# Optimization experiments

Hardware: AMD Instinct MI355X
Metric: run time of the kernel (lower is better)

## Reference

```python
import jax, jax.numpy as jnp
import numpy as np

ALPHA = 0.5
SIGMA = 1.0
THRESH = 0.1
MAX_THIN_ITERS = 128


def _gaussian_kernel(sigma):
    # scipy.ndimage.gaussian_filter default: truncate=4.0 -> radius = int(4*sigma+0.5)
    radius = int(4.0 * sigma + 0.5)
    x = np.arange(-radius, radius + 1, dtype=np.float64)
    k = np.exp(-0.5 * (x / sigma) ** 2)
    k = k / k.sum()
    return jnp.asarray(k.astype(np.float32)), radius


def _blur1d(x, k, r, axis):
    # separable Gaussian along `axis`, scipy mode='reflect' == numpy 'symmetric'
    pad = [(0, 0)] * x.ndim
    pad[axis] = (r, r)
    xp = jnp.pad(x, pad, mode='symmetric')
    n = x.shape[axis]
    out = jnp.zeros_like(x)
    for i in range(2 * r + 1):
        out = out + k[i] * jax.lax.slice_in_dim(xp, i, i + n, axis=axis)
    return out


def gaussian_blur(img, sigma):  # img: [B, H, W]
    k, r = _gaussian_kernel(sigma)
    return _blur1d(_blur1d(img, k, r, axis=1), k, r, axis=2)


def _shift(x, dy, dx):
    # neighbor value x[i+dy, j+dx] brought to [i, j], zero-padded border
    B, H, W = x.shape
    xp = jnp.pad(x, ((0, 0), (1, 1), (1, 1)))
    return xp[:, 1 + dy:1 + dy + H, 1 + dx:1 + dx + W]


def _zs_substep(img, step):
    # Zhang-Suen thinning sub-iteration; img is float {0,1} [B, H, W]
    # P2..P9 clockwise starting at north
    P = [_shift(img, -1, 0), _shift(img, -1, 1), _shift(img, 0, 1), _shift(img, 1, 1),
         _shift(img, 1, 0), _shift(img, 1, -1), _shift(img, 0, -1), _shift(img, -1, -1)]
    Bn = P[0]
    for p in P[1:]:
        Bn = Bn + p
    seq = P + [P[0]]
    A = jnp.zeros_like(img)
    for i in range(8):
        A = A + ((seq[i] < 0.5) & (seq[i + 1] > 0.5)).astype(img.dtype)
    p2, p3, p4, p5, p6, p7, p8, p9 = P
    if step == 0:
        c1 = (p2 * p4 * p6) < 0.5
        c2 = (p4 * p6 * p8) < 0.5
    else:
        c1 = (p2 * p4 * p8) < 0.5
        c2 = (p2 * p6 * p8) < 0.5
    delete = (img > 0.5) & (Bn >= 2) & (Bn <= 6) & (A == 1) & c1 & c2
    return jnp.where(delete, jnp.zeros_like(img), img)


def skeletonize(binary):  # binary float {0,1} [B, H, W] -> thinned skeleton
    def body(state):
        img, _, it = state
        img2 = _zs_substep(_zs_substep(img, 0), 1)
        return img2, jnp.any(img2 != img), it + 1

    def cond(state):
        return state[1] & (state[2] < MAX_THIN_ITERS)

    img, _, _ = jax.lax.while_loop(cond, body, (binary, jnp.array(True), jnp.array(0)))
    return img


def create_centerline_mask(gt2d, sigma=SIGMA, threshold=THRESH):  # [B, H, W]
    smooth = gaussian_blur(gt2d, sigma)
    binary = (smooth > threshold).astype(jnp.float32)
    return skeletonize(binary)


def setup_inputs() -> dict:
    key = jax.random.key(0)
    k1, k2, k3 = jax.random.split(key, 3)
    B, N, H, W = 2, 8, 512, 512
    gt = (jax.random.uniform(k2, (B, N, H, W)) > 0.9).astype(jnp.float32)
    pred = gt + 0.1 * jax.random.normal(k1, (B, N, H, W), dtype=jnp.float32)
    return {"pred_projections": pred, "gt_projections": gt}


def reference(pred_projections, gt_projections):
    B, N, H, W = pred_projections.shape
    pred = pred_projections.reshape(B * N, H, W)
    gt = gt_projections.reshape(B * N, H, W)
    # mask is built from gt only (torch detaches before CPU round-trip)
    mask = create_centerline_mask(jax.lax.stop_gradient(gt))
    diff = pred - gt
    l2_loss = jnp.mean(diff ** 2)            # == mean over per-projection mse_loss
    cl_loss = jnp.mean((diff * mask) ** 2)   # == mean over per-projection masked mse
    return ALPHA * l2_loss + (1.0 - ALPHA) * cl_loss
```

## Files before the change

kernel.cpp:

```cpp
#include <hip/hip_runtime.h>
#include <stdint.h>
#include <math.h>

static constexpr int NIMG  = 16;
static constexpr int HH    = 512;
static constexpr int WW    = 512;
static constexpr int TOTAL = NIMG * HH * WW;
static constexpr int WPR   = WW / 64;
static constexpr int QPI   = HH * WPR;
static constexpr int NQ    = TOTAL / 64;
static constexpr int MAXIT = 128;
static constexpr int SW    = 9;
static constexpr int RBLK  = 1024;

static constexpr size_t OFF_PACK = 0;
static constexpr size_t OFF_PART = (size_t)NQ * 8;

__device__ __forceinline__ void make_gk(float* gks) {
    if (threadIdx.x < 9) {
        double ssum = 0.0;
        for (int i = 0; i < 9; ++i) { double x = (double)(i - 4); ssum += exp(-0.5 * x * x); }
        double x = (double)((int)threadIdx.x - 4);
        gks[threadIdx.x] = (float)(exp(-0.5 * x * x) / ssum);
    }
}

__global__ void __launch_bounds__(256) fused_blur(const float* __restrict__ gt,
                                                  uint64_t* __restrict__ packed) {
    __shared__ float tin[72 * 72];
    __shared__ float tv[64 * 72];
    __shared__ float gks[9];
    const int tid = threadIdx.x;
    make_gk(gks);
    const int img  = blockIdx.x >> 6;
    const int tile = blockIdx.x & 63;
    const int oy = (tile >> 3) << 6, ox = (tile & 7) << 6;
    const float* G = gt + (size_t)img * (HH * WW);
    for (int i = tid; i < 72 * 72; i += 256) {
        int r = i / 72, c = i - r * 72;
        int gy = oy - 4 + r, gx = ox - 4 + c;
        gy = gy < 0 ? -gy - 1 : (gy >= HH ? 2 * HH - 1 - gy : gy);
        gx = gx < 0 ? -gx - 1 : (gx >= WW ? 2 * WW - 1 - gx : gx);
        tin[i] = G[gy * WW + gx];
    }
    __syncthreads();
    for (int i = tid; i < 64 * 72; i += 256) {
        int r = i / 72, c = i - r * 72;
        float s = 0.f;
#pragma unroll
        for (int t = 0; t < 9; ++t) s += gks[t] * tin[(r + t) * 72 + c];
        tv[i] = s;
    }
    __syncthreads();
    const int lane = tid & 63, w = tid >> 6;
    for (int j = 0; j < 16; ++j) {
        int yr = w * 16 + j;
        float s = 0.f;
#pragma unroll
        for (int t = 0; t < 9; ++t) s += gks[t] * tv[yr * 72 + lane + t];
        uint64_t m = __ballot(s > 0.1f);
        if (lane == 0) packed[(size_t)img * QPI + (oy + yr) * WPR + (ox >> 6)] = m;
    }
}

__device__ __forceinline__ void fa(uint64_t a, uint64_t b, uint64_t c, uint64_t& s, uint64_t& cy) {
    uint64_t axb = a ^ b;
    s  = axb ^ c;
    cy = (a & b) | (c & axb);
}

__device__ __forceinline__ uint64_t zs_del(uint64_t cc, uint64_t nc, uint64_t sc, uint64_t cw, uint64_t ce,
                                           uint64_t nw, uint64_t ne, uint64_t sw, uint64_t se, int step) {
    uint64_t p2 = nc;
    uint64_t p3 = (nc >> 1) | (ne << 63);
    uint64_t p4 = (cc >> 1) | (ce << 63);
    uint64_t p5 = (sc >> 1) | (se << 63);
    uint64_t p6 = sc;
    uint64_t p7 = (sc << 1) | (sw >> 63);
    uint64_t p8 = (cc << 1) | (cw >> 63);
    uint64_t p9 = (nc << 1) | (nw >> 63);

    uint64_t s1, k1, s2, k2;
    fa(p2, p3, p4, s1, k1);
    fa(p5, p6, p7, s2, k2);
    uint64_t s3 = p8 ^ p9, k3 = p8 & p9;
    uint64_t b0, k4;
    fa(s1, s2, s3, b0, k4);
    uint64_t t1, t2;
    fa(k1, k2, k3, t1, t2);
    uint64_t b1 = t1 ^ k4;
    uint64_t k5 = t1 & k4;
    uint64_t b2 = t2 ^ k5;
    uint64_t b3 = t2 & k5;
    uint64_t condB = (b1 | b2 | b3) & ~(b3 | (b0 & b1 & b2));

    uint64_t q0 = ~p2 & p3, q1 = ~p3 & p4, q2 = ~p4 & p5, q3 = ~p5 & p6;
    uint64_t q4 = ~p6 & p7, q5 = ~p7 & p8, q6 = ~p8 & p9, q7 = ~p9 & p2;
    uint64_t u1, v1, u2, v2;
    fa(q0, q1, q2, u1, v1);
    fa(q3, q4, q5, u2, v2);
    uint64_t u3 = q6 ^ q7, v3 = q6 & q7;
    uint64_t a0, v4;
    fa(u1, u2, u3, a0, v4);
    uint64_t w1, w2;
    fa(v1, v2, v3, w1, w2);
    uint64_t a1 = w1 ^ v4;
    uint64_t ka = w1 & v4;
    uint64_t a2 = w2 ^ ka;
    uint64_t a3 = w2 & ka;
    uint64_t condA = a0 & ~a1 & ~a2 & ~a3;

    uint64_t nc1, nc2;
    if (step == 0) { nc1 = ~(p2 & p4 & p6); nc2 = ~(p4 & p6 & p8); }
    else           { nc1 = ~(p2 & p4 & p8); nc2 = ~(p2 & p6 & p8); }

    return cc & condB & condA & nc1 & nc2;
}

__device__ __forceinline__ int zs_sub(const uint64_t* __restrict__ cur, uint64_t* __restrict__ nxt,
                                      int step, int wx, int y0, bool xw, bool xe) {
    int ch = 0;
    int b = y0 * SW + wx;
    uint64_t nwr, ncr, ner, cwr, ccr, cer;
    if (y0 > 0) {
        ncr = cur[b - SW];
        nwr = xw ? cur[b - SW - 1] : 0;
        ner = xe ? cur[b - SW + 1] : 0;
    } else { nwr = 0; ncr = 0; ner = 0; }
    ccr = cur[b];
    cwr = xw ? cur[b - 1] : 0;
    cer = xe ? cur[b + 1] : 0;
#pragma unroll
    for (int r = 0; r < 4; ++r) {
        uint64_t swr, scr, ser;
        if (y0 + r < HH - 1) {
            scr = cur[b + SW];
            swr = xw ? cur[b + SW - 1] : 0;
            ser = xe ? cur[b + SW + 1] : 0;
        } else { swr = 0; scr = 0; ser = 0; }
        uint64_t out = ccr;
        if (ccr) {
            uint64_t del = zs_del(ccr, ncr, scr, cwr, cer, nwr, ner, swr, ser, step);
            out = ccr & ~del;
            ch |= (del != 0ull);
        }
        nxt[b] = out;
        nwr = cwr; ncr = ccr; ner = cer;
        cwr = swr; ccr = scr; cer = ser;
        b += SW;
    }
    return ch;
}

__global__ void __launch_bounds__(1024) skel_kernel(uint64_t* __restrict__ g) {
    __shared__ uint64_t SA[HH * SW];
    __shared__ uint64_t SB[HH * SW];
    __shared__ int f2[2];
    const int tid = threadIdx.x;
    uint64_t* gimg = g + (size_t)blockIdx.x * QPI;

    for (int i = tid; i < QPI; i += 1024) SA[(i >> 3) * SW + (i & 7)] = gimg[i];
    if (tid == 0) { f2[0] = 0; f2[1] = 0; }
    __syncthreads();

    const int wx = tid & 7;
    const int y0 = (tid >> 3) * 4;
    const bool xw = wx > 0, xe = wx < WPR - 1;

    for (int it = 0; it < MAXIT; ++it) {
        const int p = it & 1;
        int ch = zs_sub(SA, SB, 0, wx, y0, xw, xe);
        __syncthreads();
        ch |= zs_sub(SB, SA, 1, wx, y0, xw, xe);
        if (__any(ch) && (tid & 63) == 0) atomicOr(&f2[p], 1);
        __syncthreads();
        int stop = (f2[p] == 0);
        if (tid == 0) f2[p ^ 1] = 0;
        if (stop) break;
    }

    for (int i = tid; i < QPI; i += 1024) gimg[i] = SA[(i >> 3) * SW + (i & 7)];
}

__global__ void __launch_bounds__(256) reduce_kernel(const float4* __restrict__ pred4, const float4* __restrict__ gt4,
                                                     const uint64_t* __restrict__ mask,
                                                     double* __restrict__ part) {
    __shared__ double sh0[256];
    __shared__ double sh1[256];
    const int tid = threadIdx.x;
    double a0 = 0.0, a1 = 0.0;
    const int N4 = TOTAL / 4;
    for (int i = blockIdx.x * 256 + tid; i < N4; i += RBLK * 256) {
        float4 pv = pred4[i];
        float4 gv = gt4[i];
        uint64_t mq = mask[i >> 4];
        int shb = (i & 15) << 2;
        double d, d2;
        d = (double)(pv.x - gv.x); d2 = d * d; a0 += d2; if ((mq >> (shb    )) & 1) a1 += d2;
        d = (double)(pv.y - gv.y); d2 = d * d; a0 += d2; if ((mq >> (shb + 1)) & 1) a1 += d2;
        d = (double)(pv.z - gv.z); d2 = d * d; a0 += d2; if ((mq >> (shb + 2)) & 1) a1 += d2;
        d = (double)(pv.w - gv.w); d2 = d * d; a0 += d2; if ((mq >> (shb + 3)) & 1) a1 += d2;
    }
    sh0[tid] = a0;
    sh1[tid] = a1;
    __syncthreads();
    for (int off = 128; off > 0; off >>= 1) {
        if (tid < off) { sh0[tid] += sh0[tid + off]; sh1[tid] += sh1[tid + off]; }
        __syncthreads();
    }
    if (tid == 0) {
        part[2 * blockIdx.x]     = sh0[0];
        part[2 * blockIdx.x + 1] = sh1[0];
    }
}

__global__ void __launch_bounds__(256) finalize_kernel(const double* __restrict__ part,
                                                       float* __restrict__ out) {
    __shared__ double sh[256];
    const int tid = threadIdx.x;
    double a = 0.0;
    for (int i = tid; i < RBLK; i += 256) a += part[2 * i] + part[2 * i + 1];
    sh[tid] = a;
    __syncthreads();
    for (int off = 128; off > 0; off >>= 1) {
        if (tid < off) sh[tid] += sh[tid + off];
        __syncthreads();
    }
    if (tid == 0) out[0] = (float)(0.5 * sh[0] / (double)TOTAL);
}

extern "C" void kernel_launch(void* const* d_in, const int* in_sizes, int n_in,
                              void* d_out, int out_size, void* d_ws, size_t ws_size,
                              hipStream_t stream) {
    const float* pred = (const float*)d_in[0];
    const float* gt   = (const float*)d_in[1];
    char* ws = (char*)d_ws;
    uint64_t* packed = (uint64_t*)(ws + OFF_PACK);
    double*   part   = (double*)(ws + OFF_PART);

    fused_blur<<<NIMG * 64, 256, 0, stream>>>(gt, packed);
    skel_kernel<<<NIMG, 1024, 0, stream>>>(packed);
    reduce_kernel<<<RBLK, 256, 0, stream>>>((const float4*)pred, (const float4*)gt, packed, part);
    finalize_kernel<<<1, 256, 0, stream>>>(part, (float*)d_out);
}
```

Before: 138.2 us.

## Fuse blur into skeleton kernel and skip inactive regions during thinning

After: 378.0 us. 173% more time.

```diff
diff --git a/kernel.cpp b/kernel.cpp
--- a/kernel.cpp
+++ b/kernel.cpp
@@ -12,6 +12,7 @@
 static constexpr int MAXIT = 128;
 static constexpr int SW    = 9;
 static constexpr int RBLK  = 1024;
+static constexpr int FW    = 10;
 
 static constexpr size_t OFF_PACK = 0;
 static constexpr size_t OFF_PART = (size_t)NQ * 8;
@@ -22,44 +23,6 @@
         for (int i = 0; i < 9; ++i) { double x = (double)(i - 4); ssum += exp(-0.5 * x * x); }
         double x = (double)((int)threadIdx.x - 4);
         gks[threadIdx.x] = (float)(exp(-0.5 * x * x) / ssum);
-    }
-}
-
-__global__ void __launch_bounds__(256) fused_blur(const float* __restrict__ gt,
-                                                  uint64_t* __restrict__ packed) {
-    __shared__ float tin[72 * 72];
-    __shared__ float tv[64 * 72];
-    __shared__ float gks[9];
-    const int tid = threadIdx.x;
-    make_gk(gks);
-    const int img  = blockIdx.x >> 6;
-    const int tile = blockIdx.x & 63;
-    const int oy = (tile >> 3) << 6, ox = (tile & 7) << 6;
-    const float* G = gt + (size_t)img * (HH * WW);
-    for (int i = tid; i < 72 * 72; i += 256) {
-        int r = i / 72, c = i - r * 72;
-        int gy = oy - 4 + r, gx = ox - 4 + c;
-        gy = gy < 0 ? -gy - 1 : (gy >= HH ? 2 * HH - 1 - gy : gy);
-        gx = gx < 0 ? -gx - 1 : (gx >= WW ? 2 * WW - 1 - gx : gx);
-        tin[i] = G[gy * WW + gx];
-    }
-    __syncthreads();
-    for (int i = tid; i < 64 * 72; i += 256) {
-        int r = i / 72, c = i - r * 72;
-        float s = 0.f;
-#pragma unroll
-        for (int t = 0; t < 9; ++t) s += gks[t] * tin[(r + t) * 72 + c];
-        tv[i] = s;
-    }
-    __syncthreads();
-    const int lane = tid & 63, w = tid >> 6;
-    for (int j = 0; j < 16; ++j) {
-        int yr = w * 16 + j;
-        float s = 0.f;
-#pragma unroll
-        for (int t = 0; t < 9; ++t) s += gks[t] * tv[yr * 72 + lane + t];
-        uint64_t m = __ballot(s > 0.1f);
-        if (lane == 0) packed[(size_t)img * QPI + (oy + yr) * WPR + (ox >> 6)] = m;
     }
 }
 
@@ -152,33 +115,88 @@
     return ch;
 }
 
-__global__ void __launch_bounds__(1024) skel_kernel(uint64_t* __restrict__ g) {
+__device__ __forceinline__ int nb_max(const int* __restrict__ lastch, int fidx) {
+    int m0 = max(max(lastch[fidx - FW - 1], lastch[fidx - FW]), lastch[fidx - FW + 1]);
+    int m1 = max(max(lastch[fidx - 1],      lastch[fidx]),      lastch[fidx + 1]);
+    int m2 = max(max(lastch[fidx + FW - 1], lastch[fidx + FW]), lastch[fidx + FW + 1]);
+    return max(max(m0, m1), m2);
+}
+
+__global__ void __launch_bounds__(1024) blur_skel(const float* __restrict__ gt,
+                                                  uint64_t* __restrict__ packed) {
     __shared__ uint64_t SA[HH * SW];
     __shared__ uint64_t SB[HH * SW];
+    __shared__ float tin[72 * 72];
+    __shared__ float tv[64 * 72];
+    __shared__ float gks[9];
+    __shared__ int lastch[130 * FW];
     __shared__ int f2[2];
     const int tid = threadIdx.x;
-    uint64_t* gimg = g + (size_t)blockIdx.x * QPI;
-
-    for (int i = tid; i < QPI; i += 1024) SA[(i >> 3) * SW + (i & 7)] = gimg[i];
+    const int img = blockIdx.x;
+    make_gk(gks);
+
+    const float* G = gt + (size_t)img * (HH * WW);
+    const int lane = tid & 63, w = tid >> 6;
+    for (int tile = 0; tile < 64; ++tile) {
+        const int oy = (tile >> 3) << 6, ox = (tile & 7) << 6;
+        for (int i = tid; i < 72 * 72; i += 1024) {
+            int r = i / 72, c = i - r * 72;
+            int gy = oy - 4 + r, gx = ox - 4 + c;
+            gy = gy < 0 ? -gy - 1 : (gy >= HH ? 2 * HH - 1 - gy : gy);
+            gx = gx < 0 ? -gx - 1 : (gx >= WW ? 2 * WW - 1 - gx : gx);
+            tin[i] = G[gy * WW + gx];
+        }
+        __syncthreads();
+        for (int i = tid; i < 64 * 72; i += 1024) {
+            int r = i / 72, c = i - r * 72;
+            float s = 0.f;
+#pragma unroll
+            for (int t = 0; t < 9; ++t) s += gks[t] * tin[(r + t) * 72 + c];
+            tv[i] = s;
+        }
+        __syncthreads();
+#pragma unroll
+        for (int jj = 0; jj < 4; ++jj) {
+            int yr = (w << 2) | jj;
+            float s = 0.f;
+#pragma unroll
+            for (int t = 0; t < 9; ++t) s += gks[t] * tv[yr * 72 + lane + t];
+            uint64_t m = __ballot(s > 0.1f);
+            if (lane == 0) SA[(oy + yr) * SW + (ox >> 6)] = m;
+        }
+        __syncthreads();
+    }
+
+    for (int i = tid; i < 130 * FW; i += 1024) lastch[i] = 0;
     if (tid == 0) { f2[0] = 0; f2[1] = 0; }
     __syncthreads();
 
     const int wx = tid & 7;
-    const int y0 = (tid >> 3) * 4;
+    const int g  = tid >> 3;
+    const int y0 = g * 4;
     const bool xw = wx > 0, xe = wx < WPR - 1;
+    const int fidx = (g + 1) * FW + wx + 1;
 
     for (int it = 0; it < MAXIT; ++it) {
-        const int p = it & 1;
-        int ch = zs_sub(SA, SB, 0, wx, y0, xw, xe);
-        __syncthreads();
-        ch |= zs_sub(SB, SA, 1, wx, y0, xw, xe);
-        if (__any(ch) && (tid & 63) == 0) atomicOr(&f2[p], 1);
+        const int p  = it & 1;
+        const int j1 = 2 * it + 1, j2 = 2 * it + 2;
+        int ch1 = 0, ch2 = 0;
+        if (nb_max(lastch, fidx) >= j1 - 2) {
+            ch1 = zs_sub(SA, SB, 0, wx, y0, xw, xe);
+            if (ch1) lastch[fidx] = j1;
+        }
+        __syncthreads();
+        if (nb_max(lastch, fidx) >= j2 - 2) {
+            ch2 = zs_sub(SB, SA, 1, wx, y0, xw, xe);
+            if (ch2) lastch[fidx] = j2;
+        }
+        if (__any(ch1 | ch2) && (tid & 63) == 0) atomicOr(&f2[p], 1);
         __syncthreads();
         int stop = (f2[p] == 0);
         if (tid == 0) f2[p ^ 1] = 0;
         if (stop) break;
     }
-
+    uint64_t* gimg = packed + (size_t)img * QPI;
     for (int i = tid; i < QPI; i += 1024) gimg[i] = SA[(i >> 3) * SW + (i & 7)];
 }
 
@@ -238,8 +256,7 @@
     uint64_t* packed = (uint64_t*)(ws + OFF_PACK);
     double*   part   = (double*)(ws + OFF_PART);
 
-    fused_blur<<<NIMG * 64, 256, 0, stream>>>(gt, packed);
-    skel_kernel<<<NIMG, 1024, 0, stream>>>(packed);
+    blur_skel<<<NIMG, 1024, 0, stream>>>(gt, packed);
     reduce_kernel<<<RBLK, 256, 0, stream>>>((const float4*)pred, (const float4*)gt, packed, part);
     finalize_kernel<<<1, 256, 0, stream>>>(part, (float*)d_out);
 }
```

## Split thinning into halo strips, fuse L2 sum into blur, sparsify masked reduce

Applied to the files above, without the earlier changes.

After: 175.0 us. +26.6%, slower.

```diff
diff --git a/kernel.cpp b/kernel.cpp
--- a/kernel.cpp
+++ b/kernel.cpp
@@ -9,12 +9,24 @@
 static constexpr int WPR   = WW / 64;
 static constexpr int QPI   = HH * WPR;
 static constexpr int NQ    = TOTAL / 64;
-static constexpr int MAXIT = 128;
 static constexpr int SW    = 9;
+static constexpr int ABLK  = 1024;
 static constexpr int RBLK  = 1024;
 
-static constexpr size_t OFF_PACK = 0;
-static constexpr size_t OFF_PART = (size_t)NQ * 8;
+static constexpr int SPI    = 4;
+static constexpr int ORS    = HH / SPI;
+static constexpr int HALO   = 16;
+static constexpr int BROWS  = ORS + 2 * HALO;
+static constexpr int BSUB   = 2 * HALO;
+static constexpr int BTHR   = (BROWS / 4) * WPR;
+static constexpr int NBLIND = NIMG * SPI;
+static constexpr int MAXIT2 = 120;
+
+static constexpr size_t OFF_PACK  = 0;
+static constexpr size_t OFF_PACK2 = (size_t)NQ * 8;
+static constexpr size_t OFF_A0    = OFF_PACK2 + (size_t)NQ * 8;
+static constexpr size_t OFF_A1    = OFF_A0 + (size_t)ABLK * 8;
+static constexpr size_t OFF_FLAG  = OFF_A1 + (size_t)RBLK * 8;
 
 __device__ __forceinline__ void make_gk(float* gks) {
     if (threadIdx.x < 9) {
@@ -25,11 +37,14 @@
     }
 }
 
-__global__ void __launch_bounds__(256) fused_blur(const float* __restrict__ gt,
-                                                  uint64_t* __restrict__ packed) {
+__global__ void __launch_bounds__(256) blur_a0(const float* __restrict__ gt,
+                                               const float4* __restrict__ pred4,
+                                               uint64_t* __restrict__ packed,
+                                               double* __restrict__ part_a0) {
     __shared__ float tin[72 * 72];
     __shared__ float tv[64 * 72];
     __shared__ float gks[9];
+    __shared__ double sh[256];
     const int tid = threadIdx.x;
     make_gk(gks);
     const int img  = blockIdx.x >> 6;
@@ -61,6 +76,24 @@
         uint64_t m = __ballot(s > 0.1f);
         if (lane == 0) packed[(size_t)img * QPI + (oy + yr) * WPR + (ox >> 6)] = m;
     }
+    double a0 = 0.0;
+    for (int i = tid; i < 1024; i += 256) {
+        int r = i >> 4, c4 = i & 15;
+        float4 pv = pred4[(size_t)img * (HH * WW / 4) + (size_t)(oy + r) * (WW / 4) + (ox >> 2) + c4];
+        const float* gv = &tin[(r + 4) * 72 + c4 * 4 + 4];
+        double d;
+        d = (double)(pv.x - gv[0]); a0 += d * d;
+        d = (double)(pv.y - gv[1]); a0 += d * d;
+        d = (double)(pv.z - gv[2]); a0 += d * d;
+        d = (double)(pv.w - gv[3]); a0 += d * d;
+    }
+    sh[tid] = a0;
+    __syncthreads();
+    for (int off = 128; off > 0; off >>= 1) {
+        if (tid < off) sh[tid] += sh[tid + off];
+        __syncthreads();
+    }
+    if (tid == 0) part_a0[blockIdx.x] = sh[0];
 }
 
 __device__ __forceinline__ void fa(uint64_t a, uint64_t b, uint64_t c, uint64_t& s, uint64_t& cy) {
@@ -115,6 +148,70 @@
     else           { nc1 = ~(p2 & p4 & p8); nc2 = ~(p2 & p6 & p8); }
 
     return cc & condB & condA & nc1 & nc2;
+}
+
+__global__ void __launch_bounds__(BTHR) skel_blind(const uint64_t* __restrict__ gin,
+                                                   uint64_t* __restrict__ gout,
+                                                   int* __restrict__ flags) {
+    __shared__ uint64_t SA[BROWS * SW];
+    __shared__ uint64_t SB[BROWS * SW];
+    __shared__ int chflag;
+    const int tid = threadIdx.x;
+    const int img = blockIdx.x / SPI;
+    const int s   = blockIdx.x % SPI;
+    const uint64_t* gi = gin + (size_t)img * QPI;
+    uint64_t* go = gout + (size_t)img * QPI;
+    const int gbase = s * ORS - HALO;
+
+    for (int i = tid; i < BROWS * WPR; i += BTHR) {
+        int lr = i >> 3, wx = i & 7;
+        int gr = gbase + lr;
+        SA[lr * SW + wx] = (gr >= 0 && gr < HH) ? gi[gr * WPR + wx] : 0;
+    }
+    if (tid == 0) chflag = 0;
+    __syncthreads();
+
+    const int wx = tid & 7;
+    const int y0 = (tid >> 3) * 4;
+    const bool xw = wx > 0, xe = wx < WPR - 1;
+    uint64_t* cur = SA;
+    uint64_t* nxt = SB;
+    int ch = 0;
+
+    for (int j = 1; j <= BSUB; ++j) {
+        if (j == BSUB - 1) ch = 0;
+        int b = y0 * SW + wx;
+        uint64_t nwr, ncr, ner;
+        if (y0 > 0) { ncr = cur[b - SW]; nwr = xw ? cur[b - SW - 1] : 0; ner = xe ? cur[b - SW + 1] : 0; }
+        else        { nwr = 0; ncr = 0; ner = 0; }
+        uint64_t ccr = cur[b], cwr = xw ? cur[b - 1] : 0, cer = xe ? cur[b + 1] : 0;
+#pragma unroll
+        for (int r = 0; r < 4; ++r) {
+            int lr = y0 + r;
+            uint64_t swr, scr, ser;
+            if (lr < BROWS - 1) { scr = cur[b + SW]; swr = xw ? cur[b + SW - 1] : 0; ser = xe ? cur[b + SW + 1] : 0; }
+            else                { swr = 0; scr = 0; ser = 0; }
+            uint64_t out = ccr;
+            if (lr > 0 && lr < BROWS - 1 && ccr) {
+                uint64_t del = zs_del(ccr, ncr, scr, cwr, cer, nwr, ner, swr, ser, (j - 1) & 1);
+                out = ccr & ~del;
+                if (del && lr >= HALO && lr < HALO + ORS) ch = 1;
+            }
+            nxt[b] = out;
+            nwr = cwr; ncr = ccr; ner = cer;
+            cwr = swr; ccr = scr; cer = ser;
+            b += SW;
+        }
+        __syncthreads();
+        uint64_t* t = cur; cur = nxt; nxt = t;
+    }
+    if (__any(ch) && (tid & 63) == 0) atomicOr(&chflag, 1);
+    for (int i = tid; i < ORS * WPR; i += BTHR) {
+        int row = i >> 3, wx2 = i & 7;
+        go[(s * ORS + row) * WPR + wx2] = cur[(HALO + row) * SW + wx2];
+    }
+    __syncthreads();
+    if (tid == 0) flags[blockIdx.x] = chflag;
 }
 
 __device__ __forceinline__ int zs_sub(const uint64_t* __restrict__ cur, uint64_t* __restrict__ nxt,
@@ -152,13 +249,19 @@
     return ch;
 }
 
-__global__ void __launch_bounds__(1024) skel_kernel(uint64_t* __restrict__ g) {
+__global__ void __launch_bounds__(1024) skel_fix(uint64_t* __restrict__ g, const int* __restrict__ flags) {
+    __shared__ int ff;
     __shared__ uint64_t SA[HH * SW];
     __shared__ uint64_t SB[HH * SW];
     __shared__ int f2[2];
     const int tid = threadIdx.x;
-    uint64_t* gimg = g + (size_t)blockIdx.x * QPI;
-
+    const int img = blockIdx.x;
+    if (tid == 0)
+        ff = flags[img * SPI] | flags[img * SPI + 1] | flags[img * SPI + 2] | flags[img * SPI + 3];
+    __syncthreads();
+    if (ff == 0) return;
+
+    uint64_t* gimg = g + (size_t)img * QPI;
     for (int i = tid; i < QPI; i += 1024) SA[(i >> 3) * SW + (i & 7)] = gimg[i];
     if (tid == 0) { f2[0] = 0; f2[1] = 0; }
     __syncthreads();
@@ -167,7 +270,7 @@
     const int y0 = (tid >> 3) * 4;
     const bool xw = wx > 0, xe = wx < WPR - 1;
 
-    for (int it = 0; it < MAXIT; ++it) {
+    for (int it = 0; it < MAXIT2; ++it) {
         const int p = it & 1;
         int ch = zs_sub(SA, SB, 0, wx, y0, xw, xe);
         __syncthreads();
@@ -178,48 +281,45 @@
         if (tid == 0) f2[p ^ 1] = 0;
         if (stop) break;
     }
-
     for (int i = tid; i < QPI; i += 1024) gimg[i] = SA[(i >> 3) * SW + (i & 7)];
 }
 
-__global__ void __launch_bounds__(256) reduce_kernel(const float4* __restrict__ pred4, const float4* __restrict__ gt4,
-                                                     const uint64_t* __restrict__ mask,
-                                                     double* __restrict__ part) {
-    __shared__ double sh0[256];
-    __shared__ double sh1[256];
-    const int tid = threadIdx.x;
-    double a0 = 0.0, a1 = 0.0;
+__global__ void __launch_bounds__(256) a1_reduce(const float4* __restrict__ pred4, const float4* __restrict__ gt4,
+                                                 const uint64_t* __restrict__ mask,
+                                                 double* __restrict__ part_a1) {
+    __shared__ double sh[256];
+    const int tid = threadIdx.x;
+    double a1 = 0.0;
     const int N4 = TOTAL / 4;
     for (int i = blockIdx.x * 256 + tid; i < N4; i += RBLK * 256) {
+        uint64_t mq = mask[i >> 4];
+        int shb = (i & 15) << 2;
+        if (!((mq >> shb) & 0xFull)) continue;
         float4 pv = pred4[i];
         float4 gv = gt4[i];
-        uint64_t mq = mask[i >> 4];
-        int shb = (i & 15) << 2;
-        double d, d2;
-        d = (double)(pv.x - gv.x); d2 = d * d; a0 += d2; if ((mq >> (shb    )) & 1) a1 += d2;
-        d = (double)(pv.y - gv.y); d2 = d * d; a0 += d2; if ((mq >> (shb + 1)) & 1) a1 += d2;
-        d = (double)(pv.z - gv.z); d2 = d * d; a0 += d2; if ((mq >> (shb + 2)) & 1) a1 += d2;
-        d = (double)(pv.w - gv.w); d2 = d * d; a0 += d2; if ((mq >> (shb + 3)) & 1) a1 += d2;
-    }
-    sh0[tid] = a0;
-    sh1[tid] = a1;
+        double d;
+        if ((mq >> (shb    )) & 1) { d = (double)(pv.x - gv.x); a1 += d * d; }
+        if ((mq >> (shb + 1)) & 1) { d = (double)(pv.y - gv.y); a1 += d * d; }
+        if ((mq >> (shb + 2)) & 1) { d = (double)(pv.z - gv.z); a1 += d * d; }
+        if ((mq >> (shb + 3)) & 1) { d = (double)(pv.w - gv.w); a1 += d * d; }
+    }
+    sh[tid] = a1;
     __syncthreads();
     for (int off = 128; off > 0; off >>= 1) {
-        if (tid < off) { sh0[tid] += sh0[tid + off]; sh1[tid] += sh1[tid + off]; }
-        __syncthreads();
-    }
-    if (tid == 0) {
-        part[2 * blockIdx.x]     = sh0[0];
-        part[2 * blockIdx.x + 1] = sh1[0];
-    }
-}
-
-__global__ void __launch_bounds__(256) finalize_kernel(const double* __restrict__ part,
+        if (tid < off) sh[tid] += sh[tid + off];
+        __syncthreads();
+    }
+    if (tid == 0) part_a1[blockIdx.x] = sh[0];
+}
+
+__global__ void __launch_bounds__(256) finalize_kernel(const double* __restrict__ part_a0,
+                                                       const double* __restrict__ part_a1,
                                                        float* __restrict__ out) {
     __shared__ double sh[256];
     const int tid = threadIdx.x;
     double a = 0.0;
-    for (int i = tid; i < RBLK; i += 256) a += part[2 * i] + part[2 * i + 1];
+    for (int i = tid; i < ABLK; i += 256) a += part_a0[i];
+    for (int i = tid; i < RBLK; i += 256) a += part_a1[i];
     sh[tid] = a;
     __syncthreads();
     for (int off = 128; off > 0; off >>= 1) {
@@ -235,11 +335,15 @@
     const float* pred = (const float*)d_in[0];
     const float* gt   = (const float*)d_in[1];
     char* ws = (char*)d_ws;
-    uint64_t* packed = (uint64_t*)(ws + OFF_PACK);
-    double*   part   = (double*)(ws + OFF_PART);
-
-    fused_blur<<<NIMG * 64, 256, 0, stream>>>(gt, packed);
-    skel_kernel<<<NIMG, 1024, 0, stream>>>(packed);
-    reduce_kernel<<<RBLK, 256, 0, stream>>>((const float4*)pred, (const float4*)gt, packed, part);
-    finalize_kernel<<<1, 256, 0, stream>>>(part, (float*)d_out);
-}
+    uint64_t* packed  = (uint64_t*)(ws + OFF_PACK);
+    uint64_t* packed2 = (uint64_t*)(ws + OFF_PACK2);
+    double*   part_a0 = (double*)(ws + OFF_A0);
+    double*   part_a1 = (double*)(ws + OFF_A1);
+    int*      flags   = (int*)(ws + OFF_FLAG);
+
+    blur_a0<<<ABLK, 256, 0, stream>>>(gt, (const float4*)pred, packed, part_a0);
+    skel_blind<<<NBLIND, BTHR, 0, stream>>>(packed, packed2, flags);
+    skel_fix<<<NIMG, 1024, 0, stream>>>(packed2, flags);
+    a1_reduce<<<RBLK, 256, 0, stream>>>((const float4*)pred, (const float4*)gt, packed2, part_a1);
+    finalize_kernel<<<1, 256, 0, stream>>>(part_a0, part_a1, (float*)d_out);
+}
```
